# Kernel tuning notes

Measured on AMD Instinct MI355X. Metric: run time of the kernel, lower is better.

The kernel has to match this reference:

```python
import jax, jax.numpy as jnp
import numpy as np

S, B, IN = 8, 8192, 2      # obs seq_len, batch, input_size
E, H, OUT, PRED = 256, 1024, 2, 12  # embed, rnn_size, output_size, pred_len


def setup_inputs() -> dict:
    key = jax.random.key(0)
    ks = jax.random.split(key, 20)
    w = lambda k, shape, fan: (jax.random.normal(k, shape, jnp.float32) / np.sqrt(fan))
    return {
        "obs_traj": jax.random.normal(ks[0], (S, B, IN), jnp.float32),
        # input embedding Linear(IN -> E)
        "W_emb": w(ks[1], (E, IN), IN), "b_emb": jnp.zeros((E,), jnp.float32),
        # LSTM layer 0: input E -> H  (torch gate order i,f,g,o)
        "W_ih0": w(ks[2], (4 * H, E), E), "W_hh0": w(ks[3], (4 * H, H), H),
        "b_ih0": jnp.zeros((4 * H,), jnp.float32), "b_hh0": jnp.zeros((4 * H,), jnp.float32),
        # LSTM layer 1: input H -> H
        "W_ih1": w(ks[4], (4 * H, H), H), "W_hh1": w(ks[5], (4 * H, H), H),
        "b_ih1": jnp.zeros((4 * H,), jnp.float32), "b_hh1": jnp.zeros((4 * H,), jnp.float32),
        # output_seq MLP: H -> 32 -> 16 -> OUT
        "W1": w(ks[6], (32, H), H), "b1": jnp.zeros((32,), jnp.float32),
        "W2": w(ks[7], (16, 32), 32), "b2": jnp.zeros((16,), jnp.float32),
        "W3": w(ks[8], (OUT, 16), 16), "b3": jnp.zeros((OUT,), jnp.float32),
    }


def reference(obs_traj, W_emb, b_emb, W_ih0, W_hh0, b_ih0, b_hh0,
              W_ih1, W_hh1, b_ih1, b_hh1, W1, b1, W2, b2, W3, b3):
    # Dropout layers are identity in eval mode.
    def embed(x):
        return jax.nn.relu(x @ W_emb.T + b_emb)

    def cell(x, h, c, Wih, Whh, bih, bhh):
        g = x @ Wih.T + h @ Whh.T + (bih + bhh)          # [B, 4H]
        i, f, gg, o = jnp.split(g, 4, axis=-1)
        c = jax.nn.sigmoid(f) * c + jax.nn.sigmoid(i) * jnp.tanh(gg)
        h = jax.nn.sigmoid(o) * jnp.tanh(c)
        return h, c

    def lstm_step(hc, x):
        h0, c0, h1, c1 = hc
        h0, c0 = cell(x, h0, c0, W_ih0, W_hh0, b_ih0, b_hh0)
        h1, c1 = cell(h0, h1, c1, W_ih1, W_hh1, b_ih1, b_hh1)
        return (h0, c0, h1, c1), h1

    def mlp(h):
        h = jax.nn.relu(h @ W1.T + b1)
        h = jax.nn.relu(h @ W2.T + b2)
        return h @ W3.T + b3

    z = jnp.zeros((B, H), obs_traj.dtype)
    hc = (z, z, z, z)

    # --- encoding: run LSTM over the observed trajectory ---
    emb_obs = embed(obs_traj)                             # [S, B, E]
    hc, _ = jax.lax.scan(lambda c, x: lstm_step(c, x), hc, emb_obs)

    curr = obs_traj[-1]                                   # [B, IN]
    curr_emb = embed(curr)

    def dec_step(carry, _):
        hc, curr, curr_emb = carry
        hc, out = lstm_step(hc, curr_emb)                 # out: [B, H]
        nxt = curr + mlp(out)                             # displacement decode
        return (hc, nxt, embed(nxt)), nxt

    _, preds = jax.lax.scan(dec_step, (hc, curr, curr_emb), None, length=PRED)
    return preds                                          # [PRED, B, OUT]
```

## Files before the change

### kernel.cpp

```cpp
#include <hip/hip_runtime.h>
#include <hip/hip_bf16.h>
#include <stdint.h>

typedef __hip_bfloat16 bf16;
typedef __attribute__((ext_vector_type(8))) short bf16x8;
typedef __attribute__((ext_vector_type(4))) float f32x4;
typedef __attribute__((ext_vector_type(8))) unsigned short us8;

#define NB 8192
#define NE 256
#define NH 1024

__device__ __forceinline__ float bf2f(unsigned short u) {
  union { unsigned int i; float f; } x; x.i = ((unsigned int)u) << 16; return x.f;
}
__device__ __forceinline__ float sigm(float x) {
  return __builtin_amdgcn_rcpf(1.f + __expf(-x));
}
__device__ __forceinline__ float tanh_f(float x) {
  return 1.f - 2.f * __builtin_amdgcn_rcpf(1.f + __expf(2.f * x));
}

#define BAR() __builtin_amdgcn_s_barrier()
#define LGKM0() do { asm volatile("s_waitcnt lgkmcnt(0)" ::: "memory"); \
                     __builtin_amdgcn_sched_barrier(0); } while (0)
#define VMW(N) asm volatile("s_waitcnt vmcnt(" #N ")" ::: "memory")

#define MFMA16(MH, AF, BV)                                                    \
  do {                                                                        \
    __builtin_amdgcn_s_setprio(1);                                            \
    _Pragma("unroll") for (int i_ = 0; i_ < 4; ++i_)                          \
      _Pragma("unroll") for (int g_ = 0; g_ < 4; ++g_)                        \
        acc[(MH)*4 + i_][g_] = __builtin_amdgcn_mfma_f32_16x16x32_bf16(       \
            AF[i_], BV[g_], acc[(MH)*4 + i_][g_], 0, 0, 0);                   \
    __builtin_amdgcn_s_setprio(0);                                            \
  } while (0)

#define LDA(BUF, MH, KK, AF)                                                  \
  do {                                                                        \
    const char* Ab_ = (const char*)&As[BUF][0][0];                            \
    _Pragma("unroll") for (int i_ = 0; i_ < 4; ++i_)                          \
      AF[i_] = *(const bf16x8*)(Ab_ +                                         \
          (wr * 128 + (MH)*64 + i_ * 16 + l15) * 128 + co##KK);               \
  } while (0)

#define LDB(BUF, KK, BV)                                                      \
  do {                                                                        \
    const char* Bb_ = (const char*)&Bs[BUF][0][0];                            \
    _Pragma("unroll") for (int g_ = 0; g_ < 4; ++g_)                          \
      BV[g_] = *(const bf16x8*)(Bb_ + (g_ * 64 + nc * 16 + l15) * 128 + co##KK); \
  } while (0)

__global__ __launch_bounds__(512) void k_cell(
    const bf16* __restrict__ X, int ldx, int Kx,
    const bf16* __restrict__ Hin, int Kh,
    const bf16* __restrict__ Wih, const bf16* __restrict__ Whh,
    const float* __restrict__ bias, float* __restrict__ Cst,
    bf16* __restrict__ Hout, int czero)
{
  __shared__ bf16 As[2][256][64];
  __shared__ bf16 Bs[2][256][64];

  const int tid = threadIdx.x;
  const int l = tid & 63;
  const int l15 = l & 15;
  const int wv = tid >> 6;
  const int wr = wv >> 2;
  const int nc = wv & 3;

  const int bid = blockIdx.x;
  const int swz = (bid & 7) * 64 + (bid >> 3);
  const int m0 = (swz & 31) * 256;
  const int hc0 = (swz >> 5) * 64;

  const int NT = (Kx + Kh) >> 6;
  const int T = NT >> 1;

  const int rowid = tid >> 3;
  const int ch = (tid & 7) ^ (rowid & 7);
  const int wv8 = wv * 8;

  const int co0 = (((l >> 4) + 0) ^ (l & 7)) * 16;
  const int co1 = (((l >> 4) + 4) ^ (l & 7)) * 16;

  f32x4 acc[8][4];
  f32x4 zero4 = {0.f, 0.f, 0.f, 0.f};
#pragma unroll
  for (int i = 0; i < 8; ++i)
#pragma unroll
    for (int j = 0; j < 4; ++j) acc[i][j] = zero4;

  auto stage_a = [&](int buf, int half, int kt) {
    int kc = kt << 6;
    const bf16* src; size_t ld;
    if (kc < Kx) { src = X + kc; ld = (size_t)ldx; }
    else         { src = Hin + (kc - Kx); ld = NH; }
#pragma unroll
    for (int rnd = 0; rnd < 2; ++rnd) {
      int tr = rnd * 128 + half * 64;
      const bf16* gp = src + (size_t)(m0 + tr + rowid) * ld + ch * 8;
      __builtin_amdgcn_global_load_lds(
          (const __attribute__((address_space(1))) void*)gp,
          (__attribute__((address_space(3))) void*)&As[buf][tr + wv8][0],
          16, 0, 0);
    }
  };
  auto stage_b = [&](int buf, int half, int kt) {
    int kc = kt << 6;
    const bf16* src; size_t ld;
    if (kc < Kx) { src = Wih + kc; ld = (size_t)Kx; }
    else         { src = Whh + (kc - Kx); ld = NH; }
#pragma unroll
    for (int rnd = 0; rnd < 2; ++rnd) {
      int gate = rnd * 2 + half;
      const bf16* gp = src + (size_t)(gate * NH + hc0 + rowid) * ld + ch * 8;
      __builtin_amdgcn_global_load_lds(
          (const __attribute__((address_space(1))) void*)gp,
          (__attribute__((address_space(3))) void*)&Bs[buf][gate * 64 + wv8][0],
          16, 0, 0);
    }
  };

  stage_a(0, 0, 0);
  stage_b(0, 0, 0);
  stage_b(0, 1, 0);
  stage_a(0, 1, 0);
  stage_b(1, 0, 1);
  VMW(4);
  BAR();

  for (int t = 0; t < T; ++t) {
    const int kt1 = 2 * t + 1;
    const bool last = (t == T - 1);
    bf16x8 af[4], bv[4];

    LDB(0, 0, bv);
    LDA(0, 0, 0, af);
    stage_b(1, 1, kt1);
    BAR(); LGKM0();
    MFMA16(0, af, bv);
    VMW(4);
    BAR();

    LDA(0, 1, 0, af);
    stage_a(1, 0, kt1);
    BAR(); LGKM0();
    MFMA16(1, af, bv);
    BAR();

    LDB(0, 1, bv);
    LDA(0, 0, 1, af);
    stage_a(1, 1, kt1);
    BAR(); LGKM0();
    MFMA16(0, af, bv);
    BAR();

    LDA(0, 1, 1, af);
    if (!last) stage_a(0, 0, kt1 + 1);
    BAR(); LGKM0();
    MFMA16(1, af, bv);
    if (last) { VMW(2); } else { VMW(4); }
    BAR();

    LDB(1, 0, bv);
    LDA(1, 0, 0, af);
    if (!last) stage_b(0, 0, kt1 + 1);
    BAR(); LGKM0();
    MFMA16(0, af, bv);
    if (last) { VMW(0); } else { VMW(4); }
    BAR();

    LDA(1, 1, 0, af);
    if (!last) stage_b(0, 1, kt1 + 1);
    BAR(); LGKM0();
    MFMA16(1, af, bv);
    BAR();

    LDB(1, 1, bv);
    LDA(1, 0, 1, af);
    if (!last) stage_a(0, 1, kt1 + 1);
    BAR(); LGKM0();
    MFMA16(0, af, bv);
    BAR();

    LDA(1, 1, 1, af);
    if (kt1 + 2 < NT) stage_b(1, 0, kt1 + 2);
    BAR(); LGKM0();
    MFMA16(1, af, bv);
    if (!last) { VMW(4); }
    BAR();
  }

  const int ecol = hc0 + nc * 16 + l15;
  const float bi = bias[ecol];
  const float bff = bias[NH + ecol];
  const float bg = bias[2 * NH + ecol];
  const float bo = bias[3 * NH + ecol];
  const int r0 = m0 + wr * 128 + ((l >> 4) << 2);
#pragma unroll
  for (int m = 0; m < 8; ++m) {
#pragma unroll
    for (int r = 0; r < 4; ++r) {
      int row = r0 + m * 16 + r;
      size_t idx = (size_t)row * NH + ecol;
      float gi = sigm(acc[m][0][r] + bi);
      float gf = sigm(acc[m][1][r] + bff);
      float gg = tanh_f(acc[m][2][r] + bg);
      float go = sigm(acc[m][3][r] + bo);
      float cold = czero ? 0.f : Cst[idx];
      float cn = gf * cold + gi * gg;
      Cst[idx] = cn;
      Hout[idx] = __float2bfloat16(go * tanh_f(cn));
    }
  }
}

__global__ __launch_bounds__(256) void k_mlp(
    const bf16* __restrict__ h1, const bf16* __restrict__ W1b, const float* __restrict__ b1,
    const float* __restrict__ W2, const float* __restrict__ b2,
    const float* __restrict__ W3, const float* __restrict__ b3,
    const float* __restrict__ cin, float* __restrict__ cout,
    float* __restrict__ preds, const float* __restrict__ Wemb,
    const float* __restrict__ bemb, bf16* __restrict__ embout)
{
  const int l = threadIdx.x & 63;
  const int row = blockIdx.x * 4 + (threadIdx.x >> 6);

  const us8* hp = (const us8*)(h1 + (size_t)row * NH + l * 16);
  us8 hv0 = hp[0], hv1 = hp[1];
  float h[16];
#pragma unroll
  for (int j = 0; j < 8; ++j) { h[j] = bf2f(hv0[j]); h[8 + j] = bf2f(hv1[j]); }

  float y1[32];
#pragma unroll
  for (int j = 0; j < 32; ++j) {
    const us8* wp = (const us8*)(W1b + (size_t)j * NH + l * 16);
    us8 w0 = wp[0], w1 = wp[1];
    float d = 0.f;
#pragma unroll
    for (int k = 0; k < 8; ++k) {
      d = fmaf(h[k], bf2f(w0[k]), d);
      d = fmaf(h[8 + k], bf2f(w1[k]), d);
    }
#pragma unroll
    for (int off2 = 32; off2 > 0; off2 >>= 1) d += __shfl_xor(d, off2);
    y1[j] = fmaxf(d + b1[j], 0.f);
  }

  float y2[16];
#pragma unroll
  for (int m = 0; m < 16; ++m) {
    float s = b2[m];
#pragma unroll
    for (int j = 0; j < 32; ++j) s = fmaf(W2[m * 32 + j], y1[j], s);
    y2[m] = fmaxf(s, 0.f);
  }
  float o0 = b3[0], o1 = b3[1];
#pragma unroll
  for (int k = 0; k < 16; ++k) {
    o0 = fmaf(W3[k], y2[k], o0);
    o1 = fmaf(W3[16 + k], y2[k], o1);
  }
  float n0 = cin[row * 2] + o0;
  float n1 = cin[row * 2 + 1] + o1;
  if (l == 0) {
    preds[row * 2] = n0; preds[row * 2 + 1] = n1;
    cout[row * 2] = n0;  cout[row * 2 + 1] = n1;
  }
#pragma unroll
  for (int q = 0; q < 4; ++q) {
    int e = l + q * 64;
    float v = fmaf(n0, Wemb[e * 2], fmaf(n1, Wemb[e * 2 + 1], bemb[e]));
    embout[(size_t)row * NE + e] = __float2bfloat16(fmaxf(v, 0.f));
  }
}

__global__ void k_embed(const float* __restrict__ x, const float* __restrict__ W,
                        const float* __restrict__ b, bf16* __restrict__ out) {
  const int l = threadIdx.x & 63;
  const int row = (blockIdx.x * 256 + threadIdx.x) >> 6;
  float x0 = x[row * 2], x1 = x[row * 2 + 1];
#pragma unroll
  for (int q = 0; q < 4; ++q) {
    int e = l + q * 64;
    float v = fmaf(x0, W[e * 2], fmaf(x1, W[e * 2 + 1], b[e]));
    out[(size_t)row * NE + e] = __float2bfloat16(fmaxf(v, 0.f));
  }
}

__global__ void k_f2b(const float* __restrict__ in, bf16* __restrict__ out, int n) {
  int i = (blockIdx.x * 256 + threadIdx.x) * 4;
  if (i >= n) return;
  float4 v = *(const float4*)(in + i);
  out[i] = __float2bfloat16(v.x);
  out[i + 1] = __float2bfloat16(v.y);
  out[i + 2] = __float2bfloat16(v.z);
  out[i + 3] = __float2bfloat16(v.w);
}

__global__ void k_badd(const float* __restrict__ a, const float* __restrict__ b,
                       float* __restrict__ o, int n) {
  int i = blockIdx.x * 256 + threadIdx.x;
  if (i < n) o[i] = a[i] + b[i];
}

extern "C" void kernel_launch(void* const* d_in, const int* in_sizes, int n_in,
                              void* d_out, int out_size, void* d_ws, size_t ws_size,
                              hipStream_t stream) {
  const float* obs   = (const float*)d_in[0];
  const float* Wemb  = (const float*)d_in[1];
  const float* bemb  = (const float*)d_in[2];
  const float* Wih0f = (const float*)d_in[3];
  const float* Whh0f = (const float*)d_in[4];
  const float* bih0  = (const float*)d_in[5];
  const float* bhh0  = (const float*)d_in[6];
  const float* Wih1f = (const float*)d_in[7];
  const float* Whh1f = (const float*)d_in[8];
  const float* bih1  = (const float*)d_in[9];
  const float* bhh1  = (const float*)d_in[10];
  const float* W1f   = (const float*)d_in[11];
  const float* b1m   = (const float*)d_in[12];
  const float* W2    = (const float*)d_in[13];
  const float* b2    = (const float*)d_in[14];
  const float* W3    = (const float*)d_in[15];
  const float* b3    = (const float*)d_in[16];

  char* ws = (char*)d_ws;
  size_t off = 0;
  auto alloc = [&](size_t bytes) -> void* {
    void* p = ws + off;
    off += (bytes + 255) & ~(size_t)255;
    return p;
  };
  bf16* wih0 = (bf16*)alloc((size_t)4096 * 256 * 2);
  bf16* whh0 = (bf16*)alloc((size_t)4096 * 1024 * 2);
  bf16* wih1 = (bf16*)alloc((size_t)4096 * 1024 * 2);
  bf16* whh1 = (bf16*)alloc((size_t)4096 * 1024 * 2);
  bf16* w1b  = (bf16*)alloc((size_t)32 * 1024 * 2);
  float* b0c = (float*)alloc((size_t)4096 * 4);
  float* b1c = (float*)alloc((size_t)4096 * 4);
  bf16* emb  = (bf16*)alloc((size_t)8 * NB * NE * 2);
  bf16* h0a  = (bf16*)alloc((size_t)NB * NH * 2);
  bf16* h0b  = (bf16*)alloc((size_t)NB * NH * 2);
  bf16* h1a  = (bf16*)alloc((size_t)NB * NH * 2);
  bf16* h1b  = (bf16*)alloc((size_t)NB * NH * 2);
  float* c0  = (float*)alloc((size_t)NB * NH * 4);
  float* c1  = (float*)alloc((size_t)NB * NH * 4);
  float* curr = (float*)alloc((size_t)NB * 2 * 4);
  bf16* cemb = (bf16*)alloc((size_t)NB * NE * 2);

  k_f2b<<<1024, 256, 0, stream>>>(Wih0f, wih0, 4096 * 256);
  k_f2b<<<4096, 256, 0, stream>>>(Whh0f, whh0, 4096 * 1024);
  k_f2b<<<4096, 256, 0, stream>>>(Wih1f, wih1, 4096 * 1024);
  k_f2b<<<4096, 256, 0, stream>>>(Whh1f, whh1, 4096 * 1024);
  k_f2b<<<32, 256, 0, stream>>>(W1f, w1b, 32 * 1024);
  k_badd<<<16, 256, 0, stream>>>(bih0, bhh0, b0c, 4096);
  k_badd<<<16, 256, 0, stream>>>(bih1, bhh1, b1c, 4096);
  k_embed<<<(8 * NB) / 4, 256, 0, stream>>>(obs, Wemb, bemb, emb);

  bf16* h0buf[2] = {h0a, h0b};
  bf16* h1buf[2] = {h1a, h1b};
  float* preds = (float*)d_out;

  for (int t = 0; t < 20; ++t) {
    const bf16* xin;
    if (t < 8)       xin = emb + (size_t)t * NB * NE;
    else if (t == 8) xin = emb + (size_t)7 * NB * NE;
    else             xin = cemb;
    int cu = t & 1, pv = cu ^ 1;
    int kh = (t == 0) ? 0 : NH;
    k_cell<<<512, 512, 0, stream>>>(xin, NE, NE, h0buf[pv], kh,
                                    wih0, whh0, b0c, c0, h0buf[cu], t == 0);
    k_cell<<<512, 512, 0, stream>>>(h0buf[cu], NH, NH, h1buf[pv], kh,
                                    wih1, whh1, b1c, c1, h1buf[cu], t == 0);
    if (t >= 8) {
      int p = t - 8;
      const float* cin = (p == 0) ? (obs + (size_t)7 * NB * 2) : curr;
      k_mlp<<<NB / 4, 256, 0, stream>>>(h1buf[cu], w1b, b1m, W2, b2, W3, b3,
                                        cin, curr, preds + (size_t)p * NB * 2,
                                        Wemb, bemb, cemb);
    }
  }
}
```

Baseline: 5.671 ms.

## Restructure GEMM main loop into 4 phases with full-K64 fragment loads

Each phase now loads both K-halves of the A and B fragments (8 bf16x8 each) and issues 32 MFMAs, which halves the number of barrier-separated phases per iteration from 8 to 4. The global-to-LDS staging order and vmcnt waits are reorganised to match. The block-to-tile swizzle is changed so each XCD gets contiguous row tiles, and launch bounds now request 2 blocks per CU. The goal is less barrier and wait overhead and better L2 locality, at the cost of more VGPRs per thread for the doubled fragments, which could cause spills under the occupancy hint.

Measured after the change: 5.001 ms. 1.13x faster.

```diff
diff --git a/kernel.cpp b/kernel.cpp
--- a/kernel.cpp
+++ b/kernel.cpp
@@ -26,32 +26,40 @@
                      __builtin_amdgcn_sched_barrier(0); } while (0)
 #define VMW(N) asm volatile("s_waitcnt vmcnt(" #N ")" ::: "memory")
 
-#define MFMA16(MH, AF, BV)                                                    \
+#define MFMA32(MH)                                                            \
   do {                                                                        \
     __builtin_amdgcn_s_setprio(1);                                            \
     _Pragma("unroll") for (int i_ = 0; i_ < 4; ++i_)                          \
-      _Pragma("unroll") for (int g_ = 0; g_ < 4; ++g_)                        \
+      _Pragma("unroll") for (int g_ = 0; g_ < 4; ++g_) {                      \
         acc[(MH)*4 + i_][g_] = __builtin_amdgcn_mfma_f32_16x16x32_bf16(       \
-            AF[i_], BV[g_], acc[(MH)*4 + i_][g_], 0, 0, 0);                   \
+            af[i_], bv[g_], acc[(MH)*4 + i_][g_], 0, 0, 0);                   \
+        acc[(MH)*4 + i_][g_] = __builtin_amdgcn_mfma_f32_16x16x32_bf16(       \
+            af[4 + i_], bv[4 + g_], acc[(MH)*4 + i_][g_], 0, 0, 0);           \
+      }                                                                       \
     __builtin_amdgcn_s_setprio(0);                                            \
   } while (0)
 
-#define LDA(BUF, MH, KK, AF)                                                  \
+#define LDA8(BUF, MH)                                                         \
   do {                                                                        \
     const char* Ab_ = (const char*)&As[BUF][0][0];                            \
-    _Pragma("unroll") for (int i_ = 0; i_ < 4; ++i_)                          \
-      AF[i_] = *(const bf16x8*)(Ab_ +                                         \
-          (wr * 128 + (MH)*64 + i_ * 16 + l15) * 128 + co##KK);               \
+    _Pragma("unroll") for (int i_ = 0; i_ < 4; ++i_) {                        \
+      int ro_ = (wr * 128 + (MH)*64 + i_ * 16 + l15) * 128;                   \
+      af[i_]     = *(const bf16x8*)(Ab_ + ro_ + co0);                         \
+      af[4 + i_] = *(const bf16x8*)(Ab_ + ro_ + co1);                         \
+    }                                                                         \
   } while (0)
 
-#define LDB(BUF, KK, BV)                                                      \
+#define LDB8(BUF)                                                             \
   do {                                                                        \
     const char* Bb_ = (const char*)&Bs[BUF][0][0];                            \
-    _Pragma("unroll") for (int g_ = 0; g_ < 4; ++g_)                          \
-      BV[g_] = *(const bf16x8*)(Bb_ + (g_ * 64 + nc * 16 + l15) * 128 + co##KK); \
+    _Pragma("unroll") for (int g_ = 0; g_ < 4; ++g_) {                        \
+      int ro_ = (g_ * 64 + nc * 16 + l15) * 128;                              \
+      bv[g_]     = *(const bf16x8*)(Bb_ + ro_ + co0);                         \
+      bv[4 + g_] = *(const bf16x8*)(Bb_ + ro_ + co1);                         \
+    }                                                                         \
   } while (0)
 
-__global__ __launch_bounds__(512) void k_cell(
+__global__ __launch_bounds__(512, 2) void k_cell(
     const bf16* __restrict__ X, int ldx, int Kx,
     const bf16* __restrict__ Hin, int Kh,
     const bf16* __restrict__ Wih, const bf16* __restrict__ Whh,
@@ -69,9 +77,9 @@
   const int nc = wv & 3;
 
   const int bid = blockIdx.x;
-  const int swz = (bid & 7) * 64 + (bid >> 3);
-  const int m0 = (swz & 31) * 256;
-  const int hc0 = (swz >> 5) * 64;
+  const int xcd = bid & 7, j = bid >> 3;
+  const int m0 = (xcd * 4 + (j & 3)) * 256;
+  const int hc0 = (j >> 2) * 64;
 
   const int NT = (Kx + Kh) >> 6;
   const int T = NT >> 1;
@@ -88,7 +96,7 @@
 #pragma unroll
   for (int i = 0; i < 8; ++i)
 #pragma unroll
-    for (int j = 0; j < 4; ++j) acc[i][j] = zero4;
+    for (int j2 = 0; j2 < 4; ++j2) acc[i][j2] = zero4;
 
   auto stage_a = [&](int buf, int half, int kt) {
     int kc = kt << 6;
@@ -122,72 +130,48 @@
   };
 
   stage_a(0, 0, 0);
+  stage_a(0, 1, 0);
   stage_b(0, 0, 0);
   stage_b(0, 1, 0);
-  stage_a(0, 1, 0);
-  stage_b(1, 0, 1);
-  VMW(4);
+  stage_a(1, 0, 1);
+  VMW(2);
   BAR();
 
   for (int t = 0; t < T; ++t) {
     const int kt1 = 2 * t + 1;
     const bool last = (t == T - 1);
-    bf16x8 af[4], bv[4];
-
-    LDB(0, 0, bv);
-    LDA(0, 0, 0, af);
+    bf16x8 af[8], bv[8];
+
+    LDB8(0); LDA8(0, 0);
+    stage_a(1, 1, kt1);
+    stage_b(1, 0, kt1);
     stage_b(1, 1, kt1);
     BAR(); LGKM0();
-    MFMA16(0, af, bv);
-    VMW(4);
+    MFMA32(0);
     BAR();
 
-    LDA(0, 1, 0, af);
-    stage_a(1, 0, kt1);
-    BAR(); LGKM0();
-    MFMA16(1, af, bv);
-    BAR();
-
-    LDB(0, 1, bv);
-    LDA(0, 0, 1, af);
-    stage_a(1, 1, kt1);
-    BAR(); LGKM0();
-    MFMA16(0, af, bv);
-    BAR();
-
-    LDA(0, 1, 1, af);
+    LDA8(0, 1);
     if (!last) stage_a(0, 0, kt1 + 1);
     BAR(); LGKM0();
-    MFMA16(1, af, bv);
-    if (last) { VMW(2); } else { VMW(4); }
+    MFMA32(1);
+    if (last) { VMW(0); } else { VMW(2); }
     BAR();
 
-    LDB(1, 0, bv);
-    LDA(1, 0, 0, af);
-    if (!last) stage_b(0, 0, kt1 + 1);
+    LDB8(1); LDA8(1, 0);
+    if (!last) {
+      stage_a(0, 1, kt1 + 1);
+      stage_b(0, 0, kt1 + 1);
+      stage_b(0, 1, kt1 + 1);
+    }
     BAR(); LGKM0();
-    MFMA16(0, af, bv);
-    if (last) { VMW(0); } else { VMW(4); }
+    MFMA32(0);
     BAR();
 
-    LDA(1, 1, 0, af);
-    if (!last) stage_b(0, 1, kt1 + 1);
+    LDA8(1, 1);
+    if (!last) stage_a(1, 0, kt1 + 2);
     BAR(); LGKM0();
-    MFMA16(1, af, bv);
-    BAR();
-
-    LDB(1, 1, bv);
-    LDA(1, 0, 1, af);
-    if (!last) stage_a(0, 1, kt1 + 1);
-    BAR(); LGKM0();
-    MFMA16(0, af, bv);
-    BAR();
-
-    LDA(1, 1, 1, af);
-    if (kt1 + 2 < NT) stage_b(1, 0, kt1 + 2);
-    BAR(); LGKM0();
-    MFMA16(1, af, bv);
-    if (!last) { VMW(4); }
+    MFMA32(1);
+    if (!last) { VMW(2); }
     BAR();
   }
 
```

## Restructure LSTM gate GEMM prefetch schedule and block-to-XCD mapping

Applied to the files above, without the earlier changes.

Reorders the global-to-LDS prefetch pipeline so each buffer half stages A and B tiles together at fewer points in the k-loop, rather than interleaving single stages between every MFMA phase. Changes the block swizzle so each XCD gets four consecutive batch-row tiles across hidden-column tiles, aiming for better L2 reuse of activations. Adds a min-blocks hint of 2 to the launch bounds, which constrains register allocation. The bunched stage calls and new wait counts risk stalls or races if the vmcnt accounting no longer matches the in-flight loads.

Result: slower. 6.088 ms (+7.4%).

```diff
diff --git a/kernel.cpp b/kernel.cpp
--- a/kernel.cpp
+++ b/kernel.cpp
@@ -26,32 +26,37 @@
                      __builtin_amdgcn_sched_barrier(0); } while (0)
 #define VMW(N) asm volatile("s_waitcnt vmcnt(" #N ")" ::: "memory")
 
-#define MFMA16(MH, AF, BV)                                                    \
+#define GLDS(G, S)                                                            \
+  __builtin_amdgcn_global_load_lds(                                           \
+      (const __attribute__((address_space(1))) void*)(G),                     \
+      (__attribute__((address_space(3))) void*)(S), 16, 0, 0)
+
+#define MFMA16S(MH)                                                           \
   do {                                                                        \
     __builtin_amdgcn_s_setprio(1);                                            \
     _Pragma("unroll") for (int i_ = 0; i_ < 4; ++i_)                          \
       _Pragma("unroll") for (int g_ = 0; g_ < 4; ++g_)                        \
         acc[(MH)*4 + i_][g_] = __builtin_amdgcn_mfma_f32_16x16x32_bf16(       \
-            AF[i_], BV[g_], acc[(MH)*4 + i_][g_], 0, 0, 0);                   \
+            af[i_], bv[g_], acc[(MH)*4 + i_][g_], 0, 0, 0);                   \
     __builtin_amdgcn_s_setprio(0);                                            \
   } while (0)
 
-#define LDA(BUF, MH, KK, AF)                                                  \
+#define LDA4(BUF, MH, CO)                                                     \
   do {                                                                        \
     const char* Ab_ = (const char*)&As[BUF][0][0];                            \
     _Pragma("unroll") for (int i_ = 0; i_ < 4; ++i_)                          \
-      AF[i_] = *(const bf16x8*)(Ab_ +                                         \
-          (wr * 128 + (MH)*64 + i_ * 16 + l15) * 128 + co##KK);               \
+      af[i_] = *(const bf16x8*)(Ab_ +                                         \
+          (wr * 128 + (MH)*64 + i_ * 16 + l15) * 128 + (CO));                 \
   } while (0)
 
-#define LDB(BUF, KK, BV)                                                      \
+#define LDB4(BUF, CO)                                                         \
   do {                                                                        \
     const char* Bb_ = (const char*)&Bs[BUF][0][0];                            \
     _Pragma("unroll") for (int g_ = 0; g_ < 4; ++g_)                          \
-      BV[g_] = *(const bf16x8*)(Bb_ + (g_ * 64 + nc * 16 + l15) * 128 + co##KK); \
+      bv[g_] = *(const bf16x8*)(Bb_ + (g_ * 64 + nc * 16 + l15) * 128 + (CO)); \
   } while (0)
 
-__global__ __launch_bounds__(512) void k_cell(
+__global__ __launch_bounds__(512, 2) void k_cell(
     const bf16* __restrict__ X, int ldx, int Kx,
     const bf16* __restrict__ Hin, int Kh,
     const bf16* __restrict__ Wih, const bf16* __restrict__ Whh,
@@ -69,9 +74,9 @@
   const int nc = wv & 3;
 
   const int bid = blockIdx.x;
-  const int swz = (bid & 7) * 64 + (bid >> 3);
-  const int m0 = (swz & 31) * 256;
-  const int hc0 = (swz >> 5) * 64;
+  const int xcd = bid & 7, j = bid >> 3;
+  const int m0 = (xcd * 4 + (j & 3)) * 256;
+  const int hc0 = (j >> 2) * 64;
 
   const int NT = (Kx + Kh) >> 6;
   const int T = NT >> 1;
@@ -88,7 +93,7 @@
 #pragma unroll
   for (int i = 0; i < 8; ++i)
 #pragma unroll
-    for (int j = 0; j < 4; ++j) acc[i][j] = zero4;
+    for (int j2 = 0; j2 < 4; ++j2) acc[i][j2] = zero4;
 
   auto stage_a = [&](int buf, int half, int kt) {
     int kc = kt << 6;
@@ -99,10 +104,7 @@
     for (int rnd = 0; rnd < 2; ++rnd) {
       int tr = rnd * 128 + half * 64;
       const bf16* gp = src + (size_t)(m0 + tr + rowid) * ld + ch * 8;
-      __builtin_amdgcn_global_load_lds(
-          (const __attribute__((address_space(1))) void*)gp,
-          (__attribute__((address_space(3))) void*)&As[buf][tr + wv8][0],
-          16, 0, 0);
+      GLDS(gp, &As[buf][tr + wv8][0]);
     }
   };
   auto stage_b = [&](int buf, int half, int kt) {
@@ -114,17 +116,15 @@
     for (int rnd = 0; rnd < 2; ++rnd) {
       int gate = rnd * 2 + half;
       const bf16* gp = src + (size_t)(gate * NH + hc0 + rowid) * ld + ch * 8;
-      __builtin_amdgcn_global_load_lds(
-          (const __attribute__((address_space(1))) void*)gp,
-          (__attribute__((address_space(3))) void*)&Bs[buf][gate * 64 + wv8][0],
-          16, 0, 0);
+      GLDS(gp, &Bs[buf][gate * 64 + wv8][0]);
     }
   };
 
   stage_a(0, 0, 0);
+  stage_a(0, 1, 0);
   stage_b(0, 0, 0);
   stage_b(0, 1, 0);
-  stage_a(0, 1, 0);
+  stage_a(1, 0, 1);
   stage_b(1, 0, 1);
   VMW(4);
   BAR();
@@ -134,59 +134,50 @@
     const bool last = (t == T - 1);
     bf16x8 af[4], bv[4];
 
-    LDB(0, 0, bv);
-    LDA(0, 0, 0, af);
+    stage_a(1, 1, kt1);
     stage_b(1, 1, kt1);
-    BAR(); LGKM0();
-    MFMA16(0, af, bv);
-    VMW(4);
-    BAR();
-
-    LDA(0, 1, 0, af);
-    stage_a(1, 0, kt1);
-    BAR(); LGKM0();
-    MFMA16(1, af, bv);
-    BAR();
-
-    LDB(0, 1, bv);
-    LDA(0, 0, 1, af);
-    stage_a(1, 1, kt1);
-    BAR(); LGKM0();
-    MFMA16(0, af, bv);
-    BAR();
-
-    LDA(0, 1, 1, af);
-    if (!last) stage_a(0, 0, kt1 + 1);
-    BAR(); LGKM0();
-    MFMA16(1, af, bv);
-    if (last) { VMW(2); } else { VMW(4); }
-    BAR();
-
-    LDB(1, 0, bv);
-    LDA(1, 0, 0, af);
-    if (!last) stage_b(0, 0, kt1 + 1);
-    BAR(); LGKM0();
-    MFMA16(0, af, bv);
+    LDB4(0, co0); LDA4(0, 0, co0);
+    BAR(); LGKM0();
+    MFMA16S(0);
+    BAR();
+
+    LDA4(0, 1, co0);
+    BAR(); LGKM0();
+    MFMA16S(1);
+    BAR();
+
+    LDB4(0, co1); LDA4(0, 0, co1);
+    BAR(); LGKM0();
+    MFMA16S(0);
+    BAR();
+
+    if (!last) { stage_a(0, 0, kt1 + 1); stage_b(0, 0, kt1 + 1); }
+    LDA4(0, 1, co1);
+    BAR(); LGKM0();
+    MFMA16S(1);
     if (last) { VMW(0); } else { VMW(4); }
     BAR();
 
-    LDA(1, 1, 0, af);
-    if (!last) stage_b(0, 1, kt1 + 1);
-    BAR(); LGKM0();
-    MFMA16(1, af, bv);
-    BAR();
-
-    LDB(1, 1, bv);
-    LDA(1, 0, 1, af);
-    if (!last) stage_a(0, 1, kt1 + 1);
-    BAR(); LGKM0();
-    MFMA16(0, af, bv);
-    BAR();
-
-    LDA(1, 1, 1, af);
-    if (kt1 + 2 < NT) stage_b(1, 0, kt1 + 2);
-    BAR(); LGKM0();
-    MFMA16(1, af, bv);
+    if (!last) { stage_a(0, 1, kt1 + 1); stage_b(0, 1, kt1 + 1); }
+    LDB4(1, co0); LDA4(1, 0, co0);
+    BAR(); LGKM0();
+    MFMA16S(0);
+    BAR();
+
+    LDA4(1, 1, co0);
+    BAR(); LGKM0();
+    MFMA16S(1);
+    BAR();
+
+    LDB4(1, co1); LDA4(1, 0, co1);
+    BAR(); LGKM0();
+    MFMA16S(0);
+    BAR();
+
+    if (!last) { stage_a(1, 0, kt1 + 2); stage_b(1, 0, kt1 + 2); }
+    LDA4(1, 1, co1);
+    BAR(); LGKM0();
+    MFMA16S(1);
     if (!last) { VMW(4); }
     BAR();
   }
```
